# Performance work log

Measured on AMD Instinct MI355X. Metric: run time of the kernel, lower is better.

## Reference

```python
import jax, jax.numpy as jnp
import numpy as np

CLIP_VAL = 32

def setup_inputs() -> dict:
    key = jax.random.key(0)
    ks = jax.random.split(key, 8)
    B, T, D_MODEL, H, DK = 4, 1024, 1024, 16, 64
    s = 0.02  # small init scale, glorot-like magnitude
    return {
        "query": jax.random.normal(ks[0], (B, T, D_MODEL), jnp.float32),
        "value": jax.random.normal(ks[1], (B, T, D_MODEL), jnp.float32),
        "W_Q": jax.random.normal(ks[2], (H, D_MODEL, DK), jnp.float32) * s,
        "W_K": jax.random.normal(ks[3], (H, D_MODEL, DK), jnp.float32) * s,
        "W_V": jax.random.normal(ks[4], (H, D_MODEL, DK), jnp.float32) * s,
        "W_O": jax.random.normal(ks[5], (H, DK, D_MODEL), jnp.float32) * s,
        "emb_Q": jax.random.normal(ks[6], (2 * CLIP_VAL + 1, DK), jnp.float32) * s,
        "emb_S": jax.random.normal(ks[7], (2 * CLIP_VAL + 1, DK), jnp.float32) * s,
    }

def reference(query, value, W_Q, W_K, W_V, W_O, emb_Q, emb_S):
    # query/value: (B, T, D_Model); per-head weights: (H, D_Model, Dk)
    T = query.shape[1]
    Dk = W_Q.shape[-1]
    sqrt_D = jnp.sqrt(jnp.asarray(Dk, query.dtype))

    # relative position index matrix: (T, T) ints in [0, 2*clip]
    tau = jnp.arange(T)
    rel = (jnp.clip(tau[None, :] - tau[:, None], -CLIP_VAL, CLIP_VAL) + CLIP_VAL)
    eQ = emb_Q[rel]  # (T, T, Dk) relative key embedding
    eS = emb_S[rel]  # (T, T, Dv) relative value embedding

    qW = jnp.einsum('btm,hmd->bhtd', query, W_Q)  # (B,H,T,Dk)
    kW = jnp.einsum('btm,hmd->bhtd', value, W_K)
    vW = jnp.einsum('btm,hmd->bhtd', value, W_V)

    # content scores + relative-query bias, both scaled by 1/sqrt(Dk)
    scores = (jnp.einsum('bhtd,bhsd->bhts', qW, kW)
              + jnp.einsum('bhtd,tsd->bhts', qW, eQ)) / sqrt_D
    p = jax.nn.softmax(scores, axis=-1)  # (B,H,T,T)

    # value combination + relative-value term
    heads = (jnp.einsum('bhts,bhsd->bhtd', p, vW)
             + jnp.einsum('bhts,tsd->bhtd', p, eS))

    # per-head output projection then sum over heads
    out = jnp.einsum('bhtd,hdm->btm', heads, W_O)  # (B,T,D_Model)
    return out
```

## Files before the change

kernel.cpp:

```cpp
#include <hip/hip_runtime.h>
#include <math.h>


typedef _Float16 f16;
typedef f16 half8 __attribute__((ext_vector_type(8)));
typedef f16 half4v __attribute__((ext_vector_type(4)));
typedef float f32x4 __attribute__((ext_vector_type(4)));
typedef float f32x16 __attribute__((ext_vector_type(16)));

__global__ __launch_bounds__(256) void prep(
    const float* __restrict__ q, const float* __restrict__ v,
    const float* __restrict__ W0, const float* __restrict__ W1,
    const float* __restrict__ W2, const float* __restrict__ WO,
    f16* __restrict__ q16, f16* __restrict__ Wt16, f16* __restrict__ WOt16) {
    __shared__ float tile[64][65];
    const int bx = blockIdx.x;
    const int t = threadIdx.x;
    if (bx < 8192) {
        int i = (bx * 256 + t) * 4;
        const float* s = (i < 4194304) ? (q + i) : (v + (i - 4194304));
        float4 x = *(const float4*)s;
        half4v h = {(f16)x.x, (f16)x.y, (f16)x.z, (f16)x.w};
        *(half4v*)&q16[i] = h;
        return;
    }
    const int c = t & 63, r4 = t >> 6;
    const int n = t >> 2, kc = (t & 3) * 16;
    if (bx < 8960) {
        const int idx = bx - 8192;
        const int z = idx >> 4, k0 = (idx & 15) * 64;
        const float* src = ((z < 16) ? W0 : (z < 32) ? W1 : W2) + (size_t)(z & 15) * 65536;
        f16* out = Wt16 + (size_t)z * 65536;
#pragma unroll
        for (int p = 0; p < 16; ++p)
            tile[r4 + p * 4][c] = src[(size_t)(k0 + r4 + p * 4) * 64 + c];
        __syncthreads();
        f16 buf[16];
#pragma unroll
        for (int i = 0; i < 16; ++i) buf[i] = (f16)tile[kc + i][n];
        *(half8*)&out[(size_t)n * 1024 + k0 + kc] = *(half8*)&buf[0];
        *(half8*)&out[(size_t)n * 1024 + k0 + kc + 8] = *(half8*)&buf[8];
        return;
    }
    {
        const int idx = bx - 8960;
        const int k0 = (idx & 15) * 64, n0 = (idx >> 4) * 64;
#pragma unroll
        for (int p = 0; p < 16; ++p)
            tile[r4 + p * 4][c] = WO[(size_t)(k0 + r4 + p * 4) * 1024 + n0 + c];
        __syncthreads();
        f16 buf[16];
#pragma unroll
        for (int i = 0; i < 16; ++i) buf[i] = (f16)tile[kc + i][n];
        *(half8*)&WOt16[(size_t)(n0 + n) * 1024 + k0 + kc] = *(half8*)&buf[0];
        *(half8*)&WOt16[(size_t)(n0 + n) * 1024 + k0 + kc + 8] = *(half8*)&buf[8];
    }
}

template <int MODE, int NT, bool DBUF>
__global__ __launch_bounds__(256) void mfma_gemm(
    const f16* __restrict__ Aq, const f16* __restrict__ Av,
    const f16* __restrict__ Bt, float* __restrict__ C,
    f16* __restrict__ oQ, f16* __restrict__ oK, f16* __restrict__ oVt) {
    constexpr int K = 1024;
    constexpr int NI = NT / 32;
    constexpr int LDSZ = (128 + NT) * 64;
    const int n0 = blockIdx.x * NT;
    const int m0 = blockIdx.y * 128;
    const f16* Abase = (MODE == 0) ? ((n0 < 1024) ? Aq : Av) : Aq;

    __shared__ f16 lds[LDSZ * (DBUF ? 2 : 1)];

    const int tid = threadIdx.x;
    const int l = tid & 63, wv = tid >> 6;
    const int rseg = l >> 3;
    const int g = (l & 7) ^ rseg;
    const bool isA = (wv < 2);
    const int rowBase = isA ? (wv & 1) * 64 : (wv & 1) * (NT / 2);
    const int nLoads = isA ? 8 : (NT / 16);
    const f16* gSrc = isA ? (Abase + (size_t)m0 * K) : (Bt + (size_t)n0 * K);
    const f16* gLane = gSrc + (size_t)(rowBase + rseg) * K + g * 8;
    const int ldsRow0 = (isA ? 0 : 128) + rowBase;

    const int fr = l & 15, fq = l >> 4, sw = fr & 7;
    const int mi2 = wv & 1, ni2 = wv >> 1;
    int aOff[NI], bOff[4];
#pragma unroll
    for (int i = 0; i < 4; ++i) bOff[i] = (mi2 * 64 + i * 16 + fr) * 128;
#pragma unroll
    for (int i = 0; i < NI; ++i)
        aOff[i] = (128 + ni2 * (NT / 2) + i * 16 + fr) * 128;

    f32x4 acc[4][NI];
#pragma unroll
    for (int i = 0; i < 4; ++i)
#pragma unroll
        for (int j = 0; j < NI; ++j) acc[i][j] = {0.f, 0.f, 0.f, 0.f};

    auto issue = [&](int k0, int buf) {
        f16* dst = lds + (buf ? LDSZ : 0);
#pragma unroll 8
        for (int i = 0; i < nLoads; ++i) {
            const f16* src = gLane + (size_t)i * 8 * K + k0;
            __builtin_amdgcn_global_load_lds(
                (const __attribute__((address_space(1))) unsigned int*)src,
                (__attribute__((address_space(3))) unsigned int*)
                    &dst[(ldsRow0 + i * 8) * 64], 16, 0, 0);
        }
    };

    if (DBUF) issue(0, 0);
    int it = 0;
    for (int k0 = 0; k0 < K; k0 += 64, ++it) {
        if (!DBUF) issue(k0, 0);
        __syncthreads();
        if (DBUF && k0 + 64 < K) issue(k0 + 64, (it + 1) & 1);
        const char* lp = (const char*)lds + (DBUF ? (it & 1) * (LDSZ * 2) : 0);
#pragma unroll
        for (int kk = 0; kk < 2; ++kk) {
            const int glq = kk * 4 + fq;
            const int sgl = (glq ^ sw) * 16;
            half8 aF[NI], bF[4];
#pragma unroll
            for (int i = 0; i < NI; ++i)
                aF[i] = *(const half8*)(lp + aOff[i] + sgl);
#pragma unroll
            for (int i = 0; i < 4; ++i)
                bF[i] = *(const half8*)(lp + bOff[i] + sgl);
#pragma unroll
            for (int mi = 0; mi < 4; ++mi)
#pragma unroll
                for (int ni = 0; ni < NI; ++ni)
                    acc[mi][ni] = __builtin_amdgcn_mfma_f32_16x16x32_f16(
                        aF[ni], bF[mi], acc[mi][ni], 0, 0, 0);
        }
        if (!DBUF) __syncthreads();
    }
#pragma unroll
    for (int mi = 0; mi < 4; ++mi) {
        const int m = m0 + mi2 * 64 + mi * 16 + fr;
#pragma unroll
        for (int ni = 0; ni < NI; ++ni) {
            const int n = n0 + ni2 * (NT / 2) + ni * 16 + 4 * fq;
            if (MODE == 1) {
                *(f32x4*)(C + (size_t)m * 1024 + n) = acc[mi][ni];
            } else {
                const int w = n >> 10, h = (n >> 6) & 15, d = n & 63;
                const int b = m >> 10, t = m & 1023;
                const size_t bh = (size_t)(b * 16 + h);
                f32x4 a = acc[mi][ni];
                if (w == 0) {
                    half4v hv = {(f16)(a[0] * 0.125f), (f16)(a[1] * 0.125f),
                                 (f16)(a[2] * 0.125f), (f16)(a[3] * 0.125f)};
                    *(half4v*)&oQ[bh * 65536 + (size_t)t * 64 + d] = hv;
                } else if (w == 1) {
                    half4v hv = {(f16)a[0], (f16)a[1], (f16)a[2], (f16)a[3]};
                    *(half4v*)&oK[bh * 65536 + (size_t)t * 64 + d] = hv;
                } else {
#pragma unroll
                    for (int r = 0; r < 4; ++r)
                        oVt[bh * 65536 + (size_t)(d + r) * 1024 + t] = (f16)a[r];
                }
            }
        }
    }
}

__global__ __launch_bounds__(512, 4) void attn_kernel(
    const f16* __restrict__ q16a, const f16* __restrict__ k16,
    const f16* __restrict__ vt16, const float* __restrict__ embQ,
    const float* __restrict__ embS, f16* __restrict__ heads16) {
    const int bh = blockIdx.x;
    const int t0 = blockIdx.y * 128;
    const f16* qg = q16a + (size_t)bh * 65536;
    const f16* kg = k16 + (size_t)bh * 65536;
    const f16* vg = vt16 + (size_t)bh * 65536;

    __shared__ __align__(16) f16 kvs[16384];
    __shared__ __align__(16) f16 qEl[66 * 136];
    __shared__ __align__(16) f16 band[128 * 72];
    __shared__ float redS[256];
    __shared__ float e64s[64];

    const int tid = threadIdx.x;
    const int wv = tid >> 6, lane = tid & 63;
    const int tl32 = lane & 31, h = lane >> 5;
    const int tcg = wv & 3, par = wv >> 2;
    const int tl = tcg * 32 + tl32;
    const int tg = t0 + tl;

    auto stageKV = [&](int i8) {
        const int j0 = i8 * 128 + par * 64;
#pragma unroll
        for (int k = 0; k < 2; ++k) {
            const int rr = tcg * 16 + k * 8;
            const int rt = rr + (lane >> 3);
            const int g = (lane & 7) ^ (rt & 7);
            __builtin_amdgcn_global_load_lds(
                (const __attribute__((address_space(1))) unsigned int*)
                    (kg + (size_t)(j0 + rt) * 64 + g * 8),
                (__attribute__((address_space(3))) unsigned int*)
                    &kvs[par * 4096 + rr * 64], 16, 0, 0);
            __builtin_amdgcn_global_load_lds(
                (const __attribute__((address_space(1))) unsigned int*)
                    (vg + (size_t)rt * 1024 + j0 + g * 8),
                (__attribute__((address_space(3))) unsigned int*)
                    &kvs[8192 + par * 4096 + rr * 64], 16, 0, 0);
        }
    };

    half8 qf[4];
#pragma unroll
    for (int ks = 0; ks < 4; ++ks)
        qf[ks] = *(const half8*)&qg[(size_t)tg * 64 + (2 * ks + h) * 8];
    stageKV(0);

    f16* embQs = band;
    for (int idx = tid; idx < 768; idx += 512) {
        const int row = idx >> 3, p = idx & 7, g = p ^ (row & 7);
        half8 hv;
        if (row < 65) {
            const float* s = embQ + row * 64 + g * 8;
#pragma unroll
            for (int j = 0; j < 8; ++j) hv[j] = (f16)s[j];
        } else {
#pragma unroll
            for (int j = 0; j < 8; ++j) hv[j] = (f16)0.f;
        }
        *(half8*)&embQs[row * 64 + p * 8] = hv;
    }
    __syncthreads();
    {
        if (par == 0) {
            f32x16 qacc[2];
#pragma unroll
            for (int mt = 0; mt < 2; ++mt)
#pragma unroll
                for (int r = 0; r < 16; ++r) qacc[mt][r] = 0.f;
#pragma unroll
            for (int ks = 0; ks < 4; ++ks)
#pragma unroll
                for (int mt = 0; mt < 2; ++mt) {
                    const int row = tl32 + 32 * mt;
                    const int p = (2 * ks + h) ^ (row & 7);
                    half8 ef = *(const half8*)&embQs[row * 64 + p * 8];
                    qacc[mt] = __builtin_amdgcn_mfma_f32_32x32x16_f16(
                        ef, qf[ks], qacc[mt], 0, 0, 0);
                }
            __syncthreads();
#pragma unroll
            for (int mt = 0; mt < 2; ++mt)
#pragma unroll
                for (int r = 0; r < 16; ++r) {
                    const int rr = (r & 3) + 8 * (r >> 2) + 4 * h + 32 * mt;
                    qEl[rr * 136 + tl] = (f16)qacc[mt][r];
                }
        } else {
            f32x16 qacc;
#pragma unroll
            for (int r = 0; r < 16; ++r) qacc[r] = 0.f;
#pragma unroll
            for (int ks = 0; ks < 4; ++ks) {
                const int row = tl32 + 64;
                const int p = (2 * ks + h) ^ (row & 7);
                half8 ef = *(const half8*)&embQs[row * 64 + p * 8];
                qacc = __builtin_amdgcn_mfma_f32_32x32x16_f16(
                    ef, qf[ks], qacc, 0, 0, 0);
            }
            __syncthreads();
#pragma unroll
            for (int r = 0; r < 16; ++r) {
                const int rr = (r & 3) + 8 * (r >> 2) + 4 * h + 64;
                if (rr < 65) qEl[rr * 136 + tl] = (f16)qacc[r];
            }
        }
    }
    for (int idx = tid; idx < 1152; idx += 512) {
        half8 hv;
#pragma unroll
        for (int j = 0; j < 8; ++j) hv[j] = (f16)(-1.0e4f);
        *(half8*)&band[idx * 8] = hv;
    }
    if (tid < 64) e64s[tid] = embS[64 * 64 + tid];
    __syncthreads();
    const float qE0 = (float)qEl[tl];
    const float qE64 = (float)qEl[64 * 136 + tl];

    float rs = 0.f, rsL = 0.f;
    f32x16 oacc[2];
#pragma unroll
    for (int dt = 0; dt < 2; ++dt)
#pragma unroll
        for (int r = 0; r < 16; ++r) oacc[dt][r] = 0.f;

#pragma unroll 1
    for (int it8 = 0; it8 < 8; ++it8) {
        const int j0 = it8 * 128 + par * 64;
        const f16* Ktc = kvs + par * 4096;
        const f16* Vtc = kvs + 8192 + par * 4096;
        f32x16 sacc[2];
#pragma unroll
        for (int mt = 0; mt < 2; ++mt)
#pragma unroll
            for (int r = 0; r < 16; ++r) sacc[mt][r] = 0.f;
#pragma unroll
        for (int ks = 0; ks < 4; ++ks)
#pragma unroll
            for (int mt = 0; mt < 2; ++mt) {
                const int row = tl32 + 32 * mt;
                const int p = (2 * ks + h) ^ (row & 7);
                half8 kf = *(const half8*)&Ktc[row * 64 + p * 8];
                sacc[mt] = __builtin_amdgcn_mfma_f32_32x32x16_f16(
                    kf, qf[ks], sacc[mt], 0, 0, 0);
            }
        const int dj = j0 - t0;
        if (dj <= -128 || dj >= 192) {
            const float bias = (dj < 0) ? qE0 : qE64;
            float ts = 0.f;
#pragma unroll
            for (int mt = 0; mt < 2; ++mt)
#pragma unroll
                for (int r = 0; r < 16; ++r) {
                    float pe = __expf(sacc[mt][r] + bias);
                    sacc[mt][r] = pe; ts += pe;
                }
            rs += ts;
            if (dj < 0) rsL += ts;
        } else {
#pragma unroll
            for (int mt = 0; mt < 2; ++mt)
#pragma unroll
                for (int r = 0; r < 16; ++r) {
                    const int sg = j0 + 32 * mt + (r & 3) + 8 * (r >> 2) + 4 * h;
                    const int ds = sg - tg;
                    const int dc = ds < -32 ? -32 : (ds > 32 ? 32 : ds);
                    float v = sacc[mt][r] + (float)qEl[(dc + 32) * 136 + tl];
                    if (ds >= -31 && ds <= 31) band[tl * 72 + ds + 31] = (f16)v;
                    float pe = __expf(v);
                    sacc[mt][r] = pe; rs += pe;
                    if (ds <= -32) rsL += pe;
                }
        }
#pragma unroll
        for (int ks = 0; ks < 4; ++ks) {
            const int mtile = ks >> 1, rb = (ks & 1) * 8;
            float ex[4];
#pragma unroll
            for (int c = 0; c < 4; ++c) {
                float send = (h == 0) ? sacc[mtile][rb + 4 + c]
                                      : sacc[mtile][rb + c];
                ex[c] = __shfl_xor(send, 32);
            }
            half8 pf;
#pragma unroll
            for (int j = 0; j < 4; ++j)
                pf[j] = (f16)((h == 0) ? sacc[mtile][rb + j] : ex[j]);
#pragma unroll
            for (int j = 0; j < 4; ++j)
                pf[4 + j] = (f16)((h == 0) ? ex[j] : sacc[mtile][rb + 4 + j]);
#pragma unroll
            for (int dt = 0; dt < 2; ++dt) {
                const int row = tl32 + 32 * dt;
                const int p = (2 * ks + h) ^ (row & 7);
                half8 vf = *(const half8*)&Vtc[row * 64 + p * 8];
                oacc[dt] = __builtin_amdgcn_mfma_f32_32x32x16_f16(
                    vf, pf, oacc[dt], 0, 0, 0);
            }
        }
        __syncthreads();
        if (it8 < 7) {
            stageKV(it8 + 1);
            __syncthreads();
        }
    }
    rs += __shfl_xor(rs, 32);
    rsL += __shfl_xor(rsL, 32);
    if (par == 1) {
        if (h == 0) { redS[tl] = rs; redS[128 + tl] = rsL; }
        float* Obuf = (float*)kvs;
#pragma unroll
        for (int dt = 0; dt < 2; ++dt)
#pragma unroll
            for (int r = 0; r < 16; ++r) {
                const int d = (r & 3) + 8 * (r >> 2) + 4 * h + 32 * dt;
                Obuf[d * 128 + tl] = oacc[dt][r];
            }
    }
    {
        const int d = tid >> 3, p = tid & 7, g = p ^ (d & 7);
        half8 hv;
#pragma unroll
        for (int j = 0; j < 8; ++j) {
            const int k = g * 8 + j;
            hv[j] = (f16)embS[((k == 63) ? 0 : (k + 1)) * 64 + d];
        }
        *(half8*)&qEl[d * 64 + p * 8] = hv;
    }
    __syncthreads();
    float sumR = 0.f, inv = 0.f;
    if (par == 0) {
        rs += redS[tl];
        rsL += redS[128 + tl];
        const float* Obuf = (const float*)kvs;
#pragma unroll
        for (int dt = 0; dt < 2; ++dt)
#pragma unroll
            for (int r = 0; r < 16; ++r) {
                const int d = (r & 3) + 8 * (r >> 2) + 4 * h + 32 * dt;
                oacc[dt][r] += Obuf[d * 128 + tl];
            }
        float sumBand = 0.f;
#pragma unroll
        for (int c = 0; c < 4; ++c) {
            const int kb = 32 * h + 8 * c;
            half8 bv = *(const half8*)&band[tl * 72 + kb];
            half8 ev;
#pragma unroll
            for (int j = 0; j < 8; ++j) {
                const int k = kb + j;
                float v;
                if (k == 63) v = rsL;
                else { v = __expf((float)bv[j]); sumBand += v; }
                ev[j] = (f16)v;
            }
            *(half8*)&band[tl * 72 + kb] = ev;
        }
        sumBand += __shfl_xor(sumBand, 32);
        sumR = rs - rsL - sumBand;
        inv = 1.0f / rs;
    }
    __syncthreads();
    if (par == 0) {
#pragma unroll
        for (int ks = 0; ks < 4; ++ks) {
            half8 pf = *(const half8*)&band[tl * 72 + 16 * ks + 8 * h];
#pragma unroll
            for (int dt = 0; dt < 2; ++dt) {
                const int row = tl32 + 32 * dt;
                const int p = (2 * ks + h) ^ (row & 7);
                half8 ef = *(const half8*)&qEl[row * 64 + p * 8];
                oacc[dt] = __builtin_amdgcn_mfma_f32_32x32x16_f16(
                    ef, pf, oacc[dt], 0, 0, 0);
            }
        }
    }
    __syncthreads();
    if (par == 0) {
        const float invv = inv;
#pragma unroll
        for (int dt = 0; dt < 2; ++dt)
#pragma unroll
            for (int r = 0; r < 16; ++r) {
                const int d = (r & 3) + 8 * (r >> 2) + 4 * h + 32 * dt;
                band[tl * 72 + d] = (f16)((oacc[dt][r] + sumR * e64s[d]) * invv);
            }
    }
    __syncthreads();
    const int b = bh >> 4, hh = bh & 15;
    const int row = tid >> 2, cb = (tid & 3) * 16;
    f16* dst = heads16 + ((size_t)(b * 1024 + t0 + row) * 1024) + hh * 64 + cb;
    *(half8*)&dst[0] = *(const half8*)&band[row * 72 + cb];
    *(half8*)&dst[8] = *(const half8*)&band[row * 72 + cb + 8];
}

extern "C" void kernel_launch(void* const* d_in, const int* in_sizes, int n_in,
                              void* d_out, int out_size, void* d_ws, size_t ws_size,
                              hipStream_t stream) {
    const float* query = (const float*)d_in[0];
    const float* value = (const float*)d_in[1];
    const float* WQ   = (const float*)d_in[2];
    const float* WK   = (const float*)d_in[3];
    const float* WV   = (const float*)d_in[4];
    const float* WO   = (const float*)d_in[5];
    const float* embQ = (const float*)d_in[6];
    const float* embS = (const float*)d_in[7];
    float* out = (float*)d_out;

    f16* w0    = (f16*)d_ws;
    f16* q16   = w0;
    f16* v16   = w0 + 4194304;
    f16* Wt16  = w0 + 8388608;
    f16* WOt16 = w0 + 11534336;
    f16* q16a  = w0 + 12582912;
    f16* k16   = w0 + 16777216;
    f16* vt16  = w0 + 20971520;
    f16* h16   = w0 + 25165824;

    prep<<<9216, 256, 0, stream>>>(query, value, WQ, WK, WV, WO,
                                   q16, Wt16, WOt16);
    mfma_gemm<0, 128, false><<<dim3(24, 32), 256, 0, stream>>>(
        q16, v16, Wt16, nullptr, q16a, k16, vt16);
    attn_kernel<<<dim3(64, 8), 512, 0, stream>>>(q16a, k16, vt16, embQ, embS, h16);
    mfma_gemm<1, 64, true><<<dim3(16, 32), 256, 0, stream>>>(
        h16, h16, WOt16, out, nullptr, nullptr, nullptr);
}
```

Before: 216.8 us.

## Halve attention query tile to 64 rows with 256-thread blocks

The attention kernel now processes 64 query rows per block with 4 waves instead of 128 rows with 8 waves, doubling the grid to 64x16 blocks. Shared buffers are shrunk and re-laid out, with qEl stride reduced and the embS table moved into the K/V staging area. The goal is more blocks for better load balance and occupancy on the GPU. The cost is that each block reloads K/V for only half the query rows, doubling K/V global traffic, and the removed unroll-1 pragma may raise register pressure.

```diff
diff --git a/kernel.cpp b/kernel.cpp
--- a/kernel.cpp
+++ b/kernel.cpp
@@ -166,46 +166,46 @@
     }
 }
 
-__global__ __launch_bounds__(512, 4) void attn_kernel(
+__global__ __launch_bounds__(256, 3) void attn_kernel(
     const f16* __restrict__ q16a, const f16* __restrict__ k16,
     const f16* __restrict__ vt16, const float* __restrict__ embQ,
     const float* __restrict__ embS, f16* __restrict__ heads16) {
     const int bh = blockIdx.x;
-    const int t0 = blockIdx.y * 128;
+    const int t0 = blockIdx.y * 64;
     const f16* qg = q16a + (size_t)bh * 65536;
     const f16* kg = k16 + (size_t)bh * 65536;
     const f16* vg = vt16 + (size_t)bh * 65536;
 
-    __shared__ __align__(16) f16 kvs[16384];
-    __shared__ __align__(16) f16 qEl[66 * 136];
-    __shared__ __align__(16) f16 band[128 * 72];
-    __shared__ float redS[256];
+    __shared__ __align__(16) f16 kv[16384];
+    __shared__ __align__(16) f16 qEl[4680];
+    __shared__ __align__(16) f16 band[4608];
+    __shared__ float redS[128];
     __shared__ float e64s[64];
 
     const int tid = threadIdx.x;
     const int wv = tid >> 6, lane = tid & 63;
     const int tl32 = lane & 31, h = lane >> 5;
-    const int tcg = wv & 3, par = wv >> 2;
+    const int tcg = wv & 1, par = wv >> 1;
     const int tl = tcg * 32 + tl32;
     const int tg = t0 + tl;
 
-    auto stageKV = [&](int i8) {
-        const int j0 = i8 * 128 + par * 64;
-#pragma unroll
-        for (int k = 0; k < 2; ++k) {
-            const int rr = tcg * 16 + k * 8;
+    auto stageKV = [&](int it8) {
+        const int j0 = it8 * 128 + par * 64;
+#pragma unroll
+        for (int k = 0; k < 4; ++k) {
+            const int rr = tcg * 32 + k * 8;
             const int rt = rr + (lane >> 3);
             const int g = (lane & 7) ^ (rt & 7);
             __builtin_amdgcn_global_load_lds(
                 (const __attribute__((address_space(1))) unsigned int*)
                     (kg + (size_t)(j0 + rt) * 64 + g * 8),
                 (__attribute__((address_space(3))) unsigned int*)
-                    &kvs[par * 4096 + rr * 64], 16, 0, 0);
+                    &kv[par * 4096 + rr * 64], 16, 0, 0);
             __builtin_amdgcn_global_load_lds(
                 (const __attribute__((address_space(1))) unsigned int*)
                     (vg + (size_t)rt * 1024 + j0 + g * 8),
                 (__attribute__((address_space(3))) unsigned int*)
-                    &kvs[8192 + par * 4096 + rr * 64], 16, 0, 0);
+                    &kv[8192 + par * 4096 + rr * 64], 16, 0, 0);
         }
     };
 
@@ -215,8 +215,7 @@
         qf[ks] = *(const half8*)&qg[(size_t)tg * 64 + (2 * ks + h) * 8];
     stageKV(0);
 
-    f16* embQs = band;
-    for (int idx = tid; idx < 768; idx += 512) {
+    for (int idx = tid; idx < 768; idx += 256) {
         const int row = idx >> 3, p = idx & 7, g = p ^ (row & 7);
         half8 hv;
         if (row < 65) {
@@ -227,55 +226,51 @@
 #pragma unroll
             for (int j = 0; j < 8; ++j) hv[j] = (f16)0.f;
         }
-        *(half8*)&embQs[row * 64 + p * 8] = hv;
+        f16* base = (row < 64) ? (band + row * 64) : (qEl + (row - 64) * 64);
+        *(half8*)&base[p * 8] = hv;
     }
     __syncthreads();
     {
+        f32x16 qacc[2];
+#pragma unroll
+        for (int mt = 0; mt < 2; ++mt)
+#pragma unroll
+            for (int r = 0; r < 16; ++r) qacc[mt][r] = 0.f;
         if (par == 0) {
-            f32x16 qacc[2];
-#pragma unroll
-            for (int mt = 0; mt < 2; ++mt)
-#pragma unroll
-                for (int r = 0; r < 16; ++r) qacc[mt][r] = 0.f;
 #pragma unroll
             for (int ks = 0; ks < 4; ++ks)
 #pragma unroll
                 for (int mt = 0; mt < 2; ++mt) {
                     const int row = tl32 + 32 * mt;
                     const int p = (2 * ks + h) ^ (row & 7);
-                    half8 ef = *(const half8*)&embQs[row * 64 + p * 8];
+                    half8 ef = *(const half8*)&band[row * 64 + p * 8];
                     qacc[mt] = __builtin_amdgcn_mfma_f32_32x32x16_f16(
                         ef, qf[ks], qacc[mt], 0, 0, 0);
                 }
-            __syncthreads();
-#pragma unroll
-            for (int mt = 0; mt < 2; ++mt)
-#pragma unroll
-                for (int r = 0; r < 16; ++r) {
-                    const int rr = (r & 3) + 8 * (r >> 2) + 4 * h + 32 * mt;
-                    qEl[rr * 136 + tl] = (f16)qacc[mt][r];
-                }
         } else {
-            f32x16 qacc;
-#pragma unroll
-            for (int r = 0; r < 16; ++r) qacc[r] = 0.f;
 #pragma unroll
             for (int ks = 0; ks < 4; ++ks) {
                 const int row = tl32 + 64;
                 const int p = (2 * ks + h) ^ (row & 7);
-                half8 ef = *(const half8*)&embQs[row * 64 + p * 8];
-                qacc = __builtin_amdgcn_mfma_f32_32x32x16_f16(
-                    ef, qf[ks], qacc, 0, 0, 0);
-            }
-            __syncthreads();
-#pragma unroll
-            for (int r = 0; r < 16; ++r) {
-                const int rr = (r & 3) + 8 * (r >> 2) + 4 * h + 64;
-                if (rr < 65) qEl[rr * 136 + tl] = (f16)qacc[r];
-            }
-        }
-    }
-    for (int idx = tid; idx < 1152; idx += 512) {
+                half8 ef = *(const half8*)&qEl[(row - 64) * 64 + p * 8];
+                qacc[0] = __builtin_amdgcn_mfma_f32_32x32x16_f16(
+                    ef, qf[ks], qacc[0], 0, 0, 0);
+            }
+        }
+        __syncthreads();
+        if (par == 0) {
+#pragma unroll
+            for (int mt = 0; mt < 2; ++mt)
+#pragma unroll
+                for (int r = 0; r < 16; ++r) {
+                    const int rr = (r & 3) + 8 * (r >> 2) + 4 * h + 32 * mt;
+                    qEl[rr * 72 + tl] = (f16)qacc[mt][r];
+                }
+        } else {
+            if (h == 0) qEl[64 * 72 + tl] = (f16)qacc[0][0];
+        }
+    }
+    for (int idx = tid; idx < 576; idx += 256) {
         half8 hv;
 #pragma unroll
         for (int j = 0; j < 8; ++j) hv[j] = (f16)(-1.0e4f);
@@ -284,7 +279,7 @@
     if (tid < 64) e64s[tid] = embS[64 * 64 + tid];
     __syncthreads();
     const float qE0 = (float)qEl[tl];
-    const float qE64 = (float)qEl[64 * 136 + tl];
+    const float qE64 = (float)qEl[64 * 72 + tl];
 
     float rs = 0.f, rsL = 0.f;
     f32x16 oacc[2];
@@ -293,11 +288,10 @@
 #pragma unroll
         for (int r = 0; r < 16; ++r) oacc[dt][r] = 0.f;
 
-#pragma unroll 1
     for (int it8 = 0; it8 < 8; ++it8) {
         const int j0 = it8 * 128 + par * 64;
-        const f16* Ktc = kvs + par * 4096;
-        const f16* Vtc = kvs + 8192 + par * 4096;
+        const f16* Ktc = kv + par * 4096;
+        const f16* Vtc = kv + 8192 + par * 4096;
         f32x16 sacc[2];
 #pragma unroll
         for (int mt = 0; mt < 2; ++mt)
@@ -314,7 +308,7 @@
                     kf, qf[ks], sacc[mt], 0, 0, 0);
             }
         const int dj = j0 - t0;
-        if (dj <= -128 || dj >= 192) {
+        if (dj <= -128 || dj >= 128) {
             const float bias = (dj < 0) ? qE0 : qE64;
             float ts = 0.f;
 #pragma unroll
@@ -334,7 +328,7 @@
                     const int sg = j0 + 32 * mt + (r & 3) + 8 * (r >> 2) + 4 * h;
                     const int ds = sg - tg;
                     const int dc = ds < -32 ? -32 : (ds > 32 ? 32 : ds);
-                    float v = sacc[mt][r] + (float)qEl[(dc + 32) * 136 + tl];
+                    float v = sacc[mt][r] + (float)qEl[(dc + 32) * 72 + tl];
                     if (ds >= -31 && ds <= 31) band[tl * 72 + ds + 31] = (f16)v;
                     float pe = __expf(v);
                     sacc[mt][r] = pe; rs += pe;
@@ -375,39 +369,39 @@
     }
     rs += __shfl_xor(rs, 32);
     rsL += __shfl_xor(rsL, 32);
+    float* Obuf = (float*)kv;
+    f16* eSt = kv + 8192;
     if (par == 1) {
-        if (h == 0) { redS[tl] = rs; redS[128 + tl] = rsL; }
-        float* Obuf = (float*)kvs;
+        if (h == 0) { redS[tl] = rs; redS[64 + tl] = rsL; }
 #pragma unroll
         for (int dt = 0; dt < 2; ++dt)
 #pragma unroll
             for (int r = 0; r < 16; ++r) {
                 const int d = (r & 3) + 8 * (r >> 2) + 4 * h + 32 * dt;
-                Obuf[d * 128 + tl] = oacc[dt][r];
-            }
-    }
-    {
-        const int d = tid >> 3, p = tid & 7, g = p ^ (d & 7);
+                Obuf[d * 64 + tl] = oacc[dt][r];
+            }
+    }
+    for (int idx = tid; idx < 512; idx += 256) {
+        const int d = idx >> 3, p = idx & 7, g = p ^ (d & 7);
         half8 hv;
 #pragma unroll
         for (int j = 0; j < 8; ++j) {
             const int k = g * 8 + j;
             hv[j] = (f16)embS[((k == 63) ? 0 : (k + 1)) * 64 + d];
         }
-        *(half8*)&qEl[d * 64 + p * 8] = hv;
+        *(half8*)&eSt[d * 64 + p * 8] = hv;
     }
     __syncthreads();
     float sumR = 0.f, inv = 0.f;
     if (par == 0) {
         rs += redS[tl];
-        rsL += redS[128 + tl];
-        const float* Obuf = (const float*)kvs;
+        rsL += redS[64 + tl];
 #pragma unroll
         for (int dt = 0; dt < 2; ++dt)
 #pragma unroll
             for (int r = 0; r < 16; ++r) {
                 const int d = (r & 3) + 8 * (r >> 2) + 4 * h + 32 * dt;
-                oacc[dt][r] += Obuf[d * 128 + tl];
+                oacc[dt][r] += Obuf[d * 64 + tl];
             }
         float sumBand = 0.f;
 #pragma unroll
@@ -438,7 +432,7 @@
             for (int dt = 0; dt < 2; ++dt) {
                 const int row = tl32 + 32 * dt;
                 const int p = (2 * ks + h) ^ (row & 7);
-                half8 ef = *(const half8*)&qEl[row * 64 + p * 8];
+                half8 ef = *(const half8*)&eSt[row * 64 + p * 8];
                 oacc[dt] = __builtin_amdgcn_mfma_f32_32x32x16_f16(
                     ef, pf, oacc[dt], 0, 0, 0);
             }
@@ -446,13 +440,12 @@
     }
     __syncthreads();
     if (par == 0) {
-        const float invv = inv;
 #pragma unroll
         for (int dt = 0; dt < 2; ++dt)
 #pragma unroll
             for (int r = 0; r < 16; ++r) {
                 const int d = (r & 3) + 8 * (r >> 2) + 4 * h + 32 * dt;
-                band[tl * 72 + d] = (f16)((oacc[dt][r] + sumR * e64s[d]) * invv);
+                band[tl * 72 + d] = (f16)((oacc[dt][r] + sumR * e64s[d]) * inv);
             }
     }
     __syncthreads();
@@ -490,7 +483,7 @@
                                    q16, Wt16, WOt16);
     mfma_gemm<0, 128, false><<<dim3(24, 32), 256, 0, stream>>>(
         q16, v16, Wt16, nullptr, q16a, k16, vt16);
-    attn_kernel<<<dim3(64, 8), 512, 0, stream>>>(q16a, k16, vt16, embQ, embS, h16);
+    attn_kernel<<<dim3(64, 16), 256, 0, stream>>>(q16a, k16, vt16, embQ, embS, h16);
     mfma_gemm<1, 64, true><<<dim3(16, 32), 256, 0, stream>>>(
         h16, h16, WOt16, out, nullptr, nullptr, nullptr);
 }
```

Result: no change. 219.7 us (+1.3%).
